# Kernel tuning notes

Hardware: AMD Instinct MI355X
Metric: run time of the kernel (lower is better)

## Reference

```python
import jax, jax.numpy as jnp
import numpy as np
from jax import lax

B_, N_, DIM, HID, DST, NT, IR, DTR, HH, WW = 16, 4096, 192, 384, 16, 17, 128, 24, 64, 64


def _selective_scan(u, delta, A, Bs, Cs, D, delta_bias):
    # u, delta: (B, Din, L); A: (Din, N); Bs, Cs: (B, N, L); D, delta_bias: (Din,)
    delta = jax.nn.softplus(delta + delta_bias[None, :, None])
    dT = jnp.moveaxis(delta, 2, 0)   # (L, B, Din)
    uT = jnp.moveaxis(u, 2, 0)       # (L, B, Din)
    BT = jnp.moveaxis(Bs, 2, 0)      # (L, B, N)
    CT = jnp.moveaxis(Cs, 2, 0)      # (L, B, N)
    Bsz, Din, L = u.shape
    Nst = A.shape[1]
    h0 = jnp.zeros((Bsz, Din, Nst), u.dtype)

    def step(h, inp):
        d_l, u_l, b_l, c_l = inp
        da = jnp.exp(d_l[:, :, None] * A[None])              # (B, Din, N)
        h = da * h + (d_l * u_l)[:, :, None] * b_l[:, None, :]
        y = jnp.einsum('bdn,bn->bd', h, c_l)
        return h, y

    _, ys = lax.scan(step, h0, (dT, uT, BT, CT))
    y = jnp.moveaxis(ys, 0, 2)                               # (B, Din, L)
    return y + u * D[None, :, None]


def _assm_forward(x, token_weight, gumbel_noise, embB, route_w1, route_b1, route_w2,
                  route_b2, inproj_w, inproj_b, cpe_w, cpe_b, x_proj_w, dt_w, dt_b,
                  A_logs, Ds, norm_g, norm_b, outproj_w, outproj_b, H, W, gather_type):
    B, n, C = x.shape
    hidden = inproj_w.shape[0]
    dst = token_weight.shape[1]
    dtr = dt_w.shape[1]

    # routing + gumbel-softmax (hard, straight-through)
    full_emb = embB @ token_weight                           # (NT, d_state)
    hmid = jax.nn.gelu(x @ route_w1.T + route_b1)
    logits = jax.nn.log_softmax(hmid @ route_w2.T + route_b2, axis=-1)
    y_soft = jax.nn.softmax(logits + gumbel_noise, axis=-1)
    idx = jnp.argmax(y_soft, axis=-1)                        # (B, n)
    y_hard = jax.nn.one_hot(idx, logits.shape[-1], dtype=y_soft.dtype)
    cls_policy = y_hard + y_soft - lax.stop_gradient(y_soft)
    prompt = cls_policy @ full_emb                           # (B, n, d_state)

    det = lax.stop_gradient(idx)
    # (gather_type 3/5 keypoint-group remap omitted: gather_type == 1 here)
    sort_idx = jnp.argsort(det, axis=-1)                     # (B, n)
    inv_idx = jnp.argsort(sort_idx, axis=-1)                 # index_reverse

    # in_proj (1x1 conv == pointwise linear) then depthwise CPE gate
    xi = x @ inproj_w.T + inproj_b                           # (B, n, hidden)
    xg = xi.reshape(B, H, W, hidden).transpose(0, 3, 1, 2)   # NCHW
    cpe = lax.conv_general_dilated(xg, cpe_w, (1, 1), 'SAME',
                                   feature_group_count=hidden,
                                   dimension_numbers=('NCHW', 'OIHW', 'NCHW'))
    cpe = cpe + cpe_b[None, :, None, None]
    xg = xg * jax.nn.sigmoid(cpe)
    xflat = xg.reshape(B, hidden, n).transpose(0, 2, 1)      # (B, n, hidden)

    sem_x = jnp.take_along_axis(xflat, sort_idx[:, :, None], axis=1)

    # Selective_Scan core
    xs = sem_x.transpose(0, 2, 1)                            # (B, Din, L)
    x_dbl = jnp.einsum('bdl,cd->bcl', xs, x_proj_w)          # (B, dtr+2N, L)
    dts, Bs, Cs = jnp.split(x_dbl, [dtr, dtr + dst], axis=1)
    dts = jnp.einsum('brl,dr->bdl', dts, dt_w)
    if gather_type != 0:
        Cs = Cs + prompt.transpose(0, 2, 1)
    A = -jnp.exp(A_logs)
    y = _selective_scan(xs, dts, A, Bs, Cs, Ds, dt_b)        # (B, Din, L)
    y = y.transpose(0, 2, 1)                                 # (B, L, hidden)

    mu = jnp.mean(y, axis=-1, keepdims=True)
    var = jnp.mean(jnp.square(y - mu), axis=-1, keepdims=True)
    yn = (y - mu) / jnp.sqrt(var + 1e-5) * norm_g + norm_b
    out = yn @ outproj_w.T + outproj_b                       # (B, n, dim)
    out = jnp.take_along_axis(out, inv_idx[:, :, None], axis=1)
    return out


def setup_inputs() -> dict:
    key = jax.random.key(0)
    ks = jax.random.split(key, 16)

    def rn(k, sh, s=0.02):
        return jax.random.normal(k, sh, dtype=jnp.float32) * s

    u = jax.random.uniform(ks[0], (B_, N_, NT), jnp.float32, 1e-6, 1.0 - 1e-6)
    gumbel = -jnp.log(-jnp.log(u))

    # faithful dt bias init (inverse-softplus of log-uniform dt)
    rng = np.random.default_rng(0)
    dt = np.exp(rng.uniform(size=HID) * (np.log(0.1) - np.log(0.001)) + np.log(0.001))
    dt = np.clip(dt, 1e-4, None)
    inv_dt = dt + np.log(-np.expm1(-dt))

    A_logs = jnp.log(jnp.tile(jnp.arange(1, DST + 1, dtype=jnp.float32), (HID, 1)))

    return {
        'x': jax.random.normal(ks[1], (B_, N_, DIM), jnp.float32),
        'token_weight': rn(ks[2], (IR, DST), 0.1),
        'gumbel_noise': gumbel,
        'embB': jax.random.uniform(ks[3], (NT, IR), jnp.float32, -1.0 / NT, 1.0 / NT),
        'route_w1': rn(ks[4], (DIM // 3, DIM)),
        'route_b1': jnp.zeros((DIM // 3,), jnp.float32),
        'route_w2': rn(ks[5], (NT, DIM // 3)),
        'route_b2': jnp.zeros((NT,), jnp.float32),
        'inproj_w': rn(ks[6], (HID, DIM)),
        'inproj_b': jnp.zeros((HID,), jnp.float32),
        'cpe_w': rn(ks[7], (HID, 1, 3, 3), 0.1),
        'cpe_b': jnp.zeros((HID,), jnp.float32),
        'x_proj_w': rn(ks[8], (DTR + 2 * DST, HID)),
        'dt_w': jax.random.uniform(ks[9], (HID, DTR), jnp.float32, -DTR ** -0.5, DTR ** -0.5),
        'dt_b': jnp.asarray(inv_dt, jnp.float32),
        'A_logs': A_logs,
        'Ds': jnp.ones((HID,), jnp.float32),
        'norm_g': jnp.ones((HID,), jnp.float32),
        'norm_b': jnp.zeros((HID,), jnp.float32),
        'outproj_w': rn(ks[10], (DIM, HID)),
        'outproj_b': jnp.zeros((DIM,), jnp.float32),
        'H': HH,
        'W': WW,
        'gather_type': 1,
    }


def reference(x, token_weight, gumbel_noise, embB, route_w1, route_b1, route_w2,
              route_b2, inproj_w, inproj_b, cpe_w, cpe_b, x_proj_w, dt_w, dt_b,
              A_logs, Ds, norm_g, norm_b, outproj_w, outproj_b, H, W, gather_type):
    return _assm_forward(x, token_weight, gumbel_noise, embB, route_w1, route_b1,
                         route_w2, route_b2, inproj_w, inproj_b, cpe_w, cpe_b,
                         x_proj_w, dt_w, dt_b, A_logs, Ds, norm_g, norm_b,
                         outproj_w, outproj_b, H, W, gather_type)
```

## Files before the change

kernel.cpp:

```cpp
#include <hip/hip_runtime.h>
#include <math.h>

#define NB 16
#define NL 4096
#define ND 192
#define NH 384
#define NS 16
#define NTK 17
#define NIR 128
#define NR 24
#define NHH 64
#define NWW 64
#define NCHUNKS 32
#define CHUNKLEN 128
#define NTOK (NB*NL)

typedef __attribute__((ext_vector_type(8))) short short8;
typedef __attribute__((ext_vector_type(4))) float floatx4;

__device__ __forceinline__ float gelu_tanh(float x){
  return 0.5f*x*(1.0f + tanhf(0.7978845608028654f*(x + 0.044715f*x*x*x)));
}
__device__ __forceinline__ float softplus_f(float x){
  return (x > 20.0f) ? x : log1pf(expf(x));
}
__device__ __forceinline__ short f2bf(float f){
  unsigned u = __float_as_uint(f);
  unsigned r = (u + 0x7fffu + ((u >> 16) & 1u)) >> 16;
  return (short)r;
}

union Pack8 { uint4 v; short s[8]; };

__global__ void k_cvtw(const float* __restrict__ inw, const float* __restrict__ ow,
                       const float* __restrict__ xpw, const float* __restrict__ dtw,
                       short* __restrict__ inwb, short* __restrict__ owb,
                       short* __restrict__ xpwb, short* __restrict__ dtwb,
                       const float* __restrict__ embB, const float* __restrict__ tw,
                       float* __restrict__ fe){
  int i = blockIdx.x*256 + threadIdx.x;
  int stride = gridDim.x*256;
  for (int p = i; p < NH*ND; p += stride) inwb[p] = f2bf(inw[p]);
  for (int p = i; p < ND*NH; p += stride) owb[p] = f2bf(ow[p]);
  for (int p = i; p < 56*NH; p += stride) xpwb[p] = f2bf(xpw[p]);
  for (int p = i; p < NH*32; p += stride){
    int r = p >> 5, c = p & 31;
    dtwb[p] = (c < NR) ? f2bf(dtw[r*NR + c]) : (short)0;
  }
  if (blockIdx.x == 0){
    for (int o = threadIdx.x; o < NTK*NS; o += 256){
      int t = o / NS, s = o % NS;
      float acc = 0.f;
      for (int k = 0; k < NIR; ++k) acc += embB[t*NIR+k]*tw[k*NS+s];
      fe[o] = acc;
    }
  }
}

template<int EPI>
__global__ __launch_bounds__(256) void k_gemm(const float* __restrict__ A, int lda,
    const float* __restrict__ W, int ldw, const float* __restrict__ bias,
    float* __restrict__ C, int ldc, int N, int K){
  __shared__ float As[16][68];
  __shared__ float Ws[16][68];
  int tid = threadIdx.x;
  int m0 = blockIdx.x*64, n0 = blockIdx.y*64;
  int tx = tid & 15, ty = tid >> 4;
  int srow = tid >> 2, skseg = (tid & 3)*4;
  float acc[4][4] = {};
  for (int k0 = 0; k0 < K; k0 += 16){
    {
      const float* ap = A + (size_t)(m0+srow)*lda + k0 + skseg;
      float4 v = *(const float4*)ap;
      As[skseg+0][srow]=v.x; As[skseg+1][srow]=v.y;
      As[skseg+2][srow]=v.z; As[skseg+3][srow]=v.w;
    }
    {
      float4 v = {0.f,0.f,0.f,0.f};
      if (n0 + srow < N) v = *(const float4*)(W + (size_t)(n0+srow)*ldw + k0 + skseg);
      Ws[skseg+0][srow]=v.x; Ws[skseg+1][srow]=v.y;
      Ws[skseg+2][srow]=v.z; Ws[skseg+3][srow]=v.w;
    }
    __syncthreads();
    #pragma unroll
    for (int kk = 0; kk < 16; ++kk){
      float4 av = *(const float4*)&As[kk][ty*4];
      float4 wv = *(const float4*)&Ws[kk][tx*4];
      acc[0][0] += av.x*wv.x; acc[0][1] += av.x*wv.y;
      acc[0][2] += av.x*wv.z; acc[0][3] += av.x*wv.w;
      acc[1][0] += av.y*wv.x; acc[1][1] += av.y*wv.y;
      acc[1][2] += av.y*wv.z; acc[1][3] += av.y*wv.w;
      acc[2][0] += av.z*wv.x; acc[2][1] += av.z*wv.y;
      acc[2][2] += av.z*wv.z; acc[2][3] += av.z*wv.w;
      acc[3][0] += av.w*wv.x; acc[3][1] += av.w*wv.y;
      acc[3][2] += av.w*wv.z; acc[3][3] += av.w*wv.w;
    }
    __syncthreads();
  }
  #pragma unroll
  for (int i = 0; i < 4; ++i){
    int m = m0 + ty*4 + i;
    #pragma unroll
    for (int j = 0; j < 4; ++j){
      int n = n0 + tx*4 + j;
      if (n < N){
        float v = acc[i][j] + (bias ? bias[n] : 0.f);
        if (EPI==1) v = gelu_tanh(v);
        C[(size_t)m*ldc + n] = v;
      }
    }
  }
}

template<int EPI, int AF32, int LNA>
__global__ __launch_bounds__(256) void k_mfma(const void* __restrict__ Aptr, int lda,
    const short* __restrict__ Wbf, int ldw, const float* __restrict__ bias,
    float* __restrict__ C, int ldc, int N, int K, const int* __restrict__ remap,
    const float* __restrict__ lnm, const float* __restrict__ lnr,
    const float* __restrict__ lng, const float* __restrict__ lnb){
  __shared__ short As[128*40];
  __shared__ short Bs[64*40];
  int tid = threadIdx.x;
  int m0 = blockIdx.x*128, n0 = blockIdx.y*64;
  int w = tid >> 6, lane = tid & 63;
  int lq = lane >> 4, lr = lane & 15;
  floatx4 acc[2][4];
  #pragma unroll
  for (int i = 0; i < 2; ++i)
    #pragma unroll
    for (int j = 0; j < 4; ++j) acc[i][j] = (floatx4){0.f,0.f,0.f,0.f};
  int ar = tid >> 1, aq = (tid & 1)*2;
  int br = tid >> 2, bq = tid & 3;
  float mr = 0.f, rr = 0.f;
  if (LNA){ mr = lnm[m0+ar]; rr = lnr[m0+ar]; }
  for (int k0 = 0; k0 < K; k0 += 32){
    Pack8 sa0, sa1;
    if (AF32){
      const float* ap = (const float*)Aptr + (size_t)(m0+ar)*lda + k0 + aq*8;
      float f[16];
      float4 f0 = *(const float4*)(ap);
      float4 f1 = *(const float4*)(ap+4);
      float4 f2 = *(const float4*)(ap+8);
      float4 f3 = *(const float4*)(ap+12);
      f[0]=f0.x; f[1]=f0.y; f[2]=f0.z; f[3]=f0.w;
      f[4]=f1.x; f[5]=f1.y; f[6]=f1.z; f[7]=f1.w;
      f[8]=f2.x; f[9]=f2.y; f[10]=f2.z; f[11]=f2.w;
      f[12]=f3.x; f[13]=f3.y; f[14]=f3.z; f[15]=f3.w;
      if (LNA){
        const float* gp = lng + k0 + aq*8;
        const float* bp = lnb + k0 + aq*8;
        #pragma unroll
        for (int j = 0; j < 16; ++j) f[j] = (f[j]-mr)*rr*gp[j] + bp[j];
      }
      #pragma unroll
      for (int j = 0; j < 8; ++j){ sa0.s[j] = f2bf(f[j]); sa1.s[j] = f2bf(f[8+j]); }
    } else {
      const short* ap = (const short*)Aptr + (size_t)(m0+ar)*lda + k0 + aq*8;
      sa0.v = *(const uint4*)ap;
      sa1.v = *(const uint4*)(ap + 8);
    }
    uint4 bv = {0u,0u,0u,0u};
    if (n0 + br < N) bv = *(const uint4*)(Wbf + (size_t)(n0+br)*ldw + k0 + bq*8);
    __syncthreads();
    *(uint4*)&As[ar*40 + aq*8]     = sa0.v;
    *(uint4*)&As[ar*40 + aq*8 + 8] = sa1.v;
    *(uint4*)&Bs[br*40 + bq*8]     = bv;
    __syncthreads();
    short8 a0 = *(const short8*)&As[(w*32      + lr)*40 + lq*8];
    short8 a1 = *(const short8*)&As[(w*32 + 16 + lr)*40 + lq*8];
    short8 b0 = *(const short8*)&Bs[(     lr)*40 + lq*8];
    short8 b1 = *(const short8*)&Bs[(16 + lr)*40 + lq*8];
    short8 b2 = *(const short8*)&Bs[(32 + lr)*40 + lq*8];
    short8 b3 = *(const short8*)&Bs[(48 + lr)*40 + lq*8];
    acc[0][0] = __builtin_amdgcn_mfma_f32_16x16x32_bf16(a0, b0, acc[0][0], 0,0,0);
    acc[0][1] = __builtin_amdgcn_mfma_f32_16x16x32_bf16(a0, b1, acc[0][1], 0,0,0);
    acc[0][2] = __builtin_amdgcn_mfma_f32_16x16x32_bf16(a0, b2, acc[0][2], 0,0,0);
    acc[0][3] = __builtin_amdgcn_mfma_f32_16x16x32_bf16(a0, b3, acc[0][3], 0,0,0);
    acc[1][0] = __builtin_amdgcn_mfma_f32_16x16x32_bf16(a1, b0, acc[1][0], 0,0,0);
    acc[1][1] = __builtin_amdgcn_mfma_f32_16x16x32_bf16(a1, b1, acc[1][1], 0,0,0);
    acc[1][2] = __builtin_amdgcn_mfma_f32_16x16x32_bf16(a1, b2, acc[1][2], 0,0,0);
    acc[1][3] = __builtin_amdgcn_mfma_f32_16x16x32_bf16(a1, b3, acc[1][3], 0,0,0);
  }
  #pragma unroll
  for (int mt = 0; mt < 2; ++mt){
    #pragma unroll
    for (int r = 0; r < 4; ++r){
      int m = m0 + w*32 + mt*16 + lq*4 + r;
      int orow = (EPI==3) ? remap[m] : m;
      #pragma unroll
      for (int nt = 0; nt < 4; ++nt){
        int n = n0 + nt*16 + lr;
        if (n < N){
          float v = acc[mt][nt][r] + (bias ? bias[n] : 0.f);
          if (EPI==2) v = softplus_f(v);
          C[(size_t)orow*ldc + n] = v;
        }
      }
    }
  }
}

__global__ __launch_bounds__(256) void k_argmax(const float* __restrict__ hmid,
    const float* __restrict__ w2, const float* __restrict__ b2,
    const float* __restrict__ gumbel, int* __restrict__ idx){
  int g = blockIdx.x*256 + threadIdx.x;
  float hm[64];
  const float4* hp = (const float4*)(hmid + (size_t)g*64);
  #pragma unroll
  for (int i = 0; i < 16; ++i){
    float4 v = hp[i];
    hm[i*4+0]=v.x; hm[i*4+1]=v.y; hm[i*4+2]=v.z; hm[i*4+3]=v.w;
  }
  float best = -INFINITY; int bi = 0;
  for (int c = 0; c < NTK; ++c){
    float s = b2[c] + gumbel[(size_t)g*NTK + c];
    #pragma unroll
    for (int j = 0; j < 64; ++j) s += hm[j]*w2[c*64+j];
    if (s > best){ best = s; bi = c; }
  }
  idx[g] = bi;
}

__global__ __launch_bounds__(256) void k_sort(const int* __restrict__ idx,
    int* __restrict__ rmap, int* __restrict__ inv){
  int b = blockIdx.x, t = threadIdx.x;
  __shared__ int hist[NTK][256];
  __shared__ int tot[NTK];
  __shared__ int keybase[NTK];
  int keys[16];
  const int* ip = idx + b*NL + t*16;
  #pragma unroll
  for (int i = 0; i < 16; ++i) keys[i] = ip[i];
  #pragma unroll
  for (int k = 0; k < NTK; ++k){
    int c = 0;
    #pragma unroll
    for (int i = 0; i < 16; ++i) c += (keys[i]==k) ? 1 : 0;
    hist[k][t] = c;
  }
  __syncthreads();
  if (t < NTK){
    int run = 0;
    for (int j = 0; j < 256; ++j){ int v = hist[t][j]; hist[t][j] = run; run += v; }
    tot[t] = run;
  }
  __syncthreads();
  if (t == 0){
    int base = 0;
    for (int k = 0; k < NTK; ++k){ keybase[k] = base; base += tot[k]; }
  }
  __syncthreads();
  #pragma unroll
  for (int i = 0; i < 16; ++i){
    int k = keys[i];
    int cb = 0;
    #pragma unroll
    for (int j = 0; j < 16; ++j) cb += (j < i && keys[j]==k) ? 1 : 0;
    int pos = keybase[k] + hist[k][t] + cb;
    rmap[b*NL + pos] = b*NL + t*16 + i;
    inv[b*NL + t*16 + i] = pos;
  }
}

__global__ __launch_bounds__(384) void k_cpe(const float* __restrict__ xi,
    const float* __restrict__ cw, const float* __restrict__ cb,
    const int* __restrict__ inv, float* __restrict__ us){
  int bl = blockIdx.x;
  int cg = bl & 3;
  int xt = (bl>>2) & 7;
  int yt = (bl>>5) & 7;
  int b  = bl >> 8;
  __shared__ float tile[10*10*96];
  int tx = threadIdx.x;
  int ty = threadIdx.y;
  int c0 = cg*96;
  int ch = c0 + tx;
  for (int yy = 0; yy < 10; ++yy){
    int gy = yt*8 + yy - 1;
    for (int xx = ty; xx < 10; xx += 4){
      int gx = xt*8 + xx - 1;
      float v = 0.f;
      if (gy >= 0 && gy < NHH && gx >= 0 && gx < NWW)
        v = xi[((size_t)(b*NL + gy*NWW + gx))*NH + ch];
      tile[(yy*10 + xx)*96 + tx] = v;
    }
  }
  float wreg[9];
  #pragma unroll
  for (int j = 0; j < 9; ++j) wreg[j] = cw[ch*9 + j];
  float bias = cb[ch];
  __syncthreads();
  for (int yy = ty; yy < 8; yy += 4){
    #pragma unroll
    for (int xx = 0; xx < 8; ++xx){
      float acc = bias;
      #pragma unroll
      for (int dy = 0; dy < 3; ++dy)
        #pragma unroll
        for (int dx = 0; dx < 3; ++dx)
          acc += tile[((yy+dy)*10 + (xx+dx))*96 + tx] * wreg[dy*3+dx];
      float center = tile[((yy+1)*10 + (xx+1))*96 + tx];
      float gate = 1.f/(1.f + expf(-acc));
      int l = (yt*8+yy)*NWW + xt*8+xx;
      int pos = inv[b*NL + l];
      us[((size_t)(b*NL + pos))*NH + ch] = center*gate;
    }
  }
}

__global__ __launch_bounds__(256) void k_bc(const float* __restrict__ dbl,
    const int* __restrict__ idx, const float* __restrict__ fe,
    const int* __restrict__ gt, float* __restrict__ Bsb, float* __restrict__ Csb,
    short* __restrict__ dtsb){
  int g = blockIdx.x*256 + threadIdx.x;
  const float* dr = dbl + (size_t)g*56;
  int id = idx[g];
  int gather = gt[0];
  #pragma unroll
  for (int n = 0; n < NR; ++n) dtsb[(size_t)g*32 + n] = f2bf(dr[n]);
  #pragma unroll
  for (int n = NR; n < 32; ++n) dtsb[(size_t)g*32 + n] = 0;
  #pragma unroll
  for (int n = 0; n < NS; ++n){
    Bsb[(size_t)g*NS + n] = dr[24+n];
    float c = dr[40+n];
    if (gather != 0) c += fe[id*NS + n];
    Csb[(size_t)g*NS + n] = c;
  }
}

__device__ __forceinline__ void decay16(bool pw, float dlt, const float* An, float* a){
  if (pw){
    float r  = __expf(dlt*An[0]);
    float r2 = r*r;
    float r3 = r2*r;
    float r4 = r2*r2;
    float r8 = r4*r4;
    float r12 = r8*r4;
    a[0]=r;     a[1]=r2;     a[2]=r3;     a[3]=r4;
    a[4]=r4*r;  a[5]=r4*r2;  a[6]=r4*r3;  a[7]=r8;
    a[8]=r8*r;  a[9]=r8*r2;  a[10]=r8*r3; a[11]=r12;
    a[12]=r12*r; a[13]=r12*r2; a[14]=r12*r3; a[15]=r8*r8;
  } else {
    #pragma unroll
    for (int n = 0; n < NS; ++n) a[n] = __expf(dlt*An[n]);
  }
}
__device__ __forceinline__ bool pwcheck(const float* An){
  bool pw = true;
  #pragma unroll
  for (int n = 1; n < NS; ++n)
    pw = pw && (fabsf(An[n] - (n+1)*An[0]) <= 1e-4f*fabsf(An[n]));
  return pw;
}

__global__ __launch_bounds__(384) void k_scan1(const float* __restrict__ delta,
    const float* __restrict__ us, const float* __restrict__ Bsb,
    const float* __restrict__ A_logs, float* __restrict__ sds, float* __restrict__ Boff){
  int bc = blockIdx.x;
  int c = bc & (NCHUNKS-1);
  int b = bc >> 5;
  int d = threadIdx.x;
  __shared__ float4 Bsh[CHUNKLEN*4];
  int base = b*NL + c*CHUNKLEN;
  {
    const float4* Bg = (const float4*)(Bsb + (size_t)base*NS);
    for (int p = d; p < CHUNKLEN*4; p += 384) Bsh[p] = Bg[p];
  }
  float An[NS];
  #pragma unroll
  for (int n = 0; n < NS; ++n) An[n] = -expf(A_logs[d*NS + n]);
  bool pw = pwcheck(An);
  float h[NS];
  #pragma unroll
  for (int n = 0; n < NS; ++n) h[n]=0.f;
  float sd = 0.f;
  __syncthreads();
  size_t gi = (size_t)base*NH + d;
  float dlt = delta[gi];
  float uv  = us[gi];
  #pragma unroll 2
  for (int s = 0; s < CHUNKLEN; ++s){
    float dltc = dlt, uvc = uv;
    if (s < CHUNKLEN-1){
      dlt = delta[gi + NH];
      uv  = us[gi + NH];
    }
    float du = dltc*uvc;
    sd += dltc;
    float a[NS];
    decay16(pw, dltc, An, a);
    float bb[NS];
    #pragma unroll
    for (int q = 0; q < 4; ++q) *(float4*)&bb[4*q] = Bsh[s*4 + q];
    #pragma unroll
    for (int n = 0; n < NS; ++n) h[n] = a[n]*h[n] + du*bb[n];
    gi += NH;
  }
  sds[(size_t)bc*NH + d] = sd;
  size_t o = ((size_t)bc*NH + d)*NS;
  *(float4*)(Boff + o)      = make_float4(h[0], h[1], h[2], h[3]);
  *(float4*)(Boff + o + 4)  = make_float4(h[4], h[5], h[6], h[7]);
  *(float4*)(Boff + o + 8)  = make_float4(h[8], h[9], h[10],h[11]);
  *(float4*)(Boff + o + 12) = make_float4(h[12],h[13],h[14],h[15]);
}

__global__ __launch_bounds__(256) void k_scan2(const float* __restrict__ A_logs,
    const float* __restrict__ sds, float* __restrict__ Boff){
  int i = blockIdx.x*256 + threadIdx.x;
  int dn = i % (NH*NS);
  int b = i / (NH*NS);
  float An = -expf(A_logs[dn]);
  int d = dn >> 4;
  float h = 0.f;
  for (int c = 0; c < NCHUNKS; ++c){
    int bc = b*NCHUNKS + c;
    float sd = sds[(size_t)bc*NH + d];
    float a = __expf(sd*An);
    size_t o = (size_t)bc*(NH*NS) + dn;
    float bo = Boff[o];
    Boff[o] = h;
    h = a*h + bo;
  }
}

__global__ __launch_bounds__(384) void k_scan3(const float* __restrict__ delta,
    const float* __restrict__ Bsb, const float* __restrict__ Csb,
    const float* __restrict__ A_logs, const float* __restrict__ Ds,
    const float* __restrict__ hinit, float* __restrict__ us){
  int bc = blockIdx.x;
  int c = bc & (NCHUNKS-1);
  int b = bc >> 5;
  int d = threadIdx.x;
  __shared__ float4 Bsh[CHUNKLEN*4];
  __shared__ float4 Csh[CHUNKLEN*4];
  int base = b*NL + c*CHUNKLEN;
  {
    const float4* Bg = (const float4*)(Bsb + (size_t)base*NS);
    const float4* Cg = (const float4*)(Csb + (size_t)base*NS);
    for (int p = d; p < CHUNKLEN*4; p += 384){
      Bsh[p] = Bg[p];
      Csh[p] = Cg[p];
    }
  }
  float An[NS];
  #pragma unroll
  for (int n = 0; n < NS; ++n) An[n] = -expf(A_logs[d*NS + n]);
  bool pw = pwcheck(An);
  float h[NS];
  size_t ho = ((size_t)bc*NH + d)*NS;
  {
    float4 h0 = *(const float4*)(hinit + ho);
    float4 h1 = *(const float4*)(hinit + ho + 4);
    float4 h2 = *(const float4*)(hinit + ho + 8);
    float4 h3 = *(const float4*)(hinit + ho + 12);
    h[0]=h0.x; h[1]=h0.y; h[2]=h0.z; h[3]=h0.w;
    h[4]=h1.x; h[5]=h1.y; h[6]=h1.z; h[7]=h1.w;
    h[8]=h2.x; h[9]=h2.y; h[10]=h2.z; h[11]=h2.w;
    h[12]=h3.x; h[13]=h3.y; h[14]=h3.z; h[15]=h3.w;
  }
  float Dd = Ds[d];
  __syncthreads();
  size_t gi = (size_t)base*NH + d;
  float dlt = delta[gi];
  float uv  = us[gi];
  #pragma unroll 2
  for (int s = 0; s < CHUNKLEN; ++s){
    float dltc = dlt, uvc = uv;
    if (s < CHUNKLEN-1){
      dlt = delta[gi + NH];
      uv  = us[gi + NH];
    }
    float du = dltc*uvc;
    float a[NS];
    decay16(pw, dltc, An, a);
    float bb[NS], cc[NS];
    #pragma unroll
    for (int q = 0; q < 4; ++q){
      *(float4*)&bb[4*q] = Bsh[s*4 + q];
      *(float4*)&cc[4*q] = Csh[s*4 + q];
    }
    #pragma unroll
    for (int n = 0; n < NS; ++n) h[n] = a[n]*h[n] + du*bb[n];
    float ya = 0.f, yb = 0.f, yc = 0.f, yd = 0.f;
    #pragma unroll
    for (int q = 0; q < 4; ++q){
      ya += h[q]*cc[q];
      yb += h[4+q]*cc[4+q];
      yc += h[8+q]*cc[8+q];
      yd += h[12+q]*cc[12+q];
    }
    float y = (ya+yb)+(yc+yd);
    us[gi] = y + uvc*Dd;
    gi += NH;
  }
}

__global__ __launch_bounds__(256) void k_lnstat(const float* __restrict__ y,
    float* __restrict__ mean, float* __restrict__ rstd){
  int g = blockIdx.x*4 + (threadIdx.x >> 6);
  int lane = threadIdx.x & 63;
  size_t ro = (size_t)g*NH;
  float v[6];
  #pragma unroll
  for (int i = 0; i < 6; ++i) v[i] = y[ro + i*64 + lane];
  float s = 0.f;
  #pragma unroll
  for (int i = 0; i < 6; ++i) s += v[i];
  #pragma unroll
  for (int off = 32; off > 0; off >>= 1) s += __shfl_xor(s, off);
  float mu = s * (1.f/NH);
  float vs = 0.f;
  #pragma unroll
  for (int i = 0; i < 6; ++i){ float d = v[i]-mu; vs += d*d; }
  #pragma unroll
  for (int off = 32; off > 0; off >>= 1) vs += __shfl_xor(vs, off);
  float rs = rsqrtf(vs*(1.f/NH) + 1e-5f);
  if (lane == 0){ mean[g] = mu; rstd[g] = rs; }
}

extern "C" void kernel_launch(void* const* d_in, const int* in_sizes, int n_in,
                              void* d_out, int out_size, void* d_ws, size_t ws_size,
                              hipStream_t stream){
  const float* x      = (const float*)d_in[0];
  const float* tw     = (const float*)d_in[1];
  const float* gumbel = (const float*)d_in[2];
  const float* embB   = (const float*)d_in[3];
  const float* rw1    = (const float*)d_in[4];
  const float* rb1    = (const float*)d_in[5];
  const float* rw2    = (const float*)d_in[6];
  const float* rb2    = (const float*)d_in[7];
  const float* inw    = (const float*)d_in[8];
  const float* inb    = (const float*)d_in[9];
  const float* cw     = (const float*)d_in[10];
  const float* cb     = (const float*)d_in[11];
  const float* xpw    = (const float*)d_in[12];
  const float* dtw    = (const float*)d_in[13];
  const float* dtb    = (const float*)d_in[14];
  const float* A_logs = (const float*)d_in[15];
  const float* Ds     = (const float*)d_in[16];
  const float* ng     = (const float*)d_in[17];
  const float* nbv    = (const float*)d_in[18];
  const float* ow     = (const float*)d_in[19];
  const float* ob     = (const float*)d_in[20];
  const int*   gt     = (const int*)d_in[23];
  float* out = (float*)d_out;

  float* ws = (float*)d_ws;
  size_t o = 0;
  float* fe   = ws + o; o += 512;
  int* idx    = (int*)(ws + o); o += NTOK;
  int* rmap   = (int*)(ws + o); o += NTOK;
  int* inv    = (int*)(ws + o); o += NTOK;
  float* hmid = ws + o; o += (size_t)NTOK*64;
  float* xi   = ws + o; o += (size_t)NTOK*NH;
  float* us   = ws + o; o += (size_t)NTOK*NH;
  float* Bsb  = ws + o; o += (size_t)NTOK*NS;
  float* Csb  = ws + o; o += (size_t)NTOK*NS;
  float* sds  = ws + o; o += (size_t)NB*NCHUNKS*NH;
  float* Bof  = ws + o; o += (size_t)NB*NCHUNKS*NH*NS;
  short* inwb = (short*)(ws + o); o += (NH*ND)/2;
  short* owb  = (short*)(ws + o); o += (ND*NH)/2;
  short* xpwb = (short*)(ws + o); o += (56*NH)/2 + 32;
  short* dtwb = (short*)(ws + o); o += (NH*32)/2;
  float* dbl = hmid;
  float* delta = xi;
  short* dtsb = (short*)Bof;
  float* lnmean = (float*)idx;
  float* lnrstd = (float*)inv;

  k_cvtw<<<64,256,0,stream>>>(inw, ow, xpw, dtw, inwb, owb, xpwb, dtwb, embB, tw, fe);
  k_gemm<1><<<dim3(NTOK/64,1),256,0,stream>>>(x, ND, rw1, ND, rb1, hmid, 64, 64, ND);
  k_argmax<<<NTOK/256,256,0,stream>>>(hmid, rw2, rb2, gumbel, idx);
  k_sort<<<NB,256,0,stream>>>(idx, rmap, inv);
  k_mfma<0,1,0><<<dim3(NTOK/128,6),256,0,stream>>>(x, ND, inwb, ND, inb, xi, NH, NH, ND,
      nullptr, nullptr, nullptr, nullptr, nullptr);
  k_cpe<<<NB*64*4,dim3(96,4),0,stream>>>(xi, cw, cb, inv, us);
  k_mfma<0,1,0><<<dim3(NTOK/128,1),256,0,stream>>>(us, NH, xpwb, NH, nullptr, dbl, 56, 56, NH,
      nullptr, nullptr, nullptr, nullptr, nullptr);
  k_bc<<<NTOK/256,256,0,stream>>>(dbl, idx, fe, gt, Bsb, Csb, dtsb);
  k_mfma<2,0,0><<<dim3(NTOK/128,6),256,0,stream>>>(dtsb, 32, dtwb, 32, dtb, delta, NH, NH, 32,
      nullptr, nullptr, nullptr, nullptr, nullptr);
  k_scan1<<<NB*NCHUNKS,384,0,stream>>>(delta, us, Bsb, A_logs, sds, Bof);
  k_scan2<<<(NB*NH*NS)/256,256,0,stream>>>(A_logs, sds, Bof);
  k_scan3<<<NB*NCHUNKS,384,0,stream>>>(delta, Bsb, Csb, A_logs, Ds, Bof, us);
  k_lnstat<<<NTOK/4,256,0,stream>>>(us, lnmean, lnrstd);
  k_mfma<3,1,1><<<dim3(NTOK/128,3),256,0,stream>>>(us, NH, owb, NH, ob, out, ND, ND, NH,
      rmap, lnmean, lnrstd, ng, nbv);
}
```

Baseline: 726.8 us.

## Fuse x_proj GEMM with B/C split and LayerNorm stats into scan

Replaces the generic x_proj MFMA GEMM plus the separate k_bc split kernel with one kernel that computes the 56-wide projection and writes dt (bf16), B and C (with the prompt embedding added) straight from the accumulators. It also moves the per-token LayerNorm mean/rstd computation into the tail of k_scan3, re-reading each chunk's freshly written rows after a block barrier. This removes two launches and the round trip of the intermediate dbl buffer. In exchange, k_scan3 gets a serial stats phase that runs on only 512 blocks, and the fused GEMM epilogue does scattered small stores.

```diff
diff --git a/kernel.cpp b/kernel.cpp
--- a/kernel.cpp
+++ b/kernel.cpp
@@ -200,6 +200,87 @@
   }
 }
 
+__global__ __launch_bounds__(256) void k_xdbl(const float* __restrict__ us,
+    const short* __restrict__ xpwb, const int* __restrict__ idx,
+    const float* __restrict__ fe, const int* __restrict__ gt,
+    float* __restrict__ Bsb, float* __restrict__ Csb, short* __restrict__ dtsb){
+  __shared__ short As[128*40];
+  __shared__ short Bs[64*40];
+  int tid = threadIdx.x;
+  int m0 = blockIdx.x*128;
+  int w = tid >> 6, lane = tid & 63;
+  int lq = lane >> 4, lr = lane & 15;
+  floatx4 acc[2][4];
+  #pragma unroll
+  for (int i = 0; i < 2; ++i)
+    #pragma unroll
+    for (int j = 0; j < 4; ++j) acc[i][j] = (floatx4){0.f,0.f,0.f,0.f};
+  int ar = tid >> 1, aq = (tid & 1)*2;
+  int br = tid >> 2, bq = tid & 3;
+  for (int k0 = 0; k0 < NH; k0 += 32){
+    Pack8 sa0, sa1;
+    {
+      const float* ap = us + (size_t)(m0+ar)*NH + k0 + aq*8;
+      float f[16];
+      float4 f0 = *(const float4*)(ap);
+      float4 f1 = *(const float4*)(ap+4);
+      float4 f2 = *(const float4*)(ap+8);
+      float4 f3 = *(const float4*)(ap+12);
+      f[0]=f0.x; f[1]=f0.y; f[2]=f0.z; f[3]=f0.w;
+      f[4]=f1.x; f[5]=f1.y; f[6]=f1.z; f[7]=f1.w;
+      f[8]=f2.x; f[9]=f2.y; f[10]=f2.z; f[11]=f2.w;
+      f[12]=f3.x; f[13]=f3.y; f[14]=f3.z; f[15]=f3.w;
+      #pragma unroll
+      for (int j = 0; j < 8; ++j){ sa0.s[j] = f2bf(f[j]); sa1.s[j] = f2bf(f[8+j]); }
+    }
+    uint4 bv = {0u,0u,0u,0u};
+    if (br < 56) bv = *(const uint4*)(xpwb + (size_t)br*NH + k0 + bq*8);
+    __syncthreads();
+    *(uint4*)&As[ar*40 + aq*8]     = sa0.v;
+    *(uint4*)&As[ar*40 + aq*8 + 8] = sa1.v;
+    *(uint4*)&Bs[br*40 + bq*8]     = bv;
+    __syncthreads();
+    short8 a0 = *(const short8*)&As[(w*32      + lr)*40 + lq*8];
+    short8 a1 = *(const short8*)&As[(w*32 + 16 + lr)*40 + lq*8];
+    short8 b0 = *(const short8*)&Bs[(     lr)*40 + lq*8];
+    short8 b1 = *(const short8*)&Bs[(16 + lr)*40 + lq*8];
+    short8 b2 = *(const short8*)&Bs[(32 + lr)*40 + lq*8];
+    short8 b3 = *(const short8*)&Bs[(48 + lr)*40 + lq*8];
+    acc[0][0] = __builtin_amdgcn_mfma_f32_16x16x32_bf16(a0, b0, acc[0][0], 0,0,0);
+    acc[0][1] = __builtin_amdgcn_mfma_f32_16x16x32_bf16(a0, b1, acc[0][1], 0,0,0);
+    acc[0][2] = __builtin_amdgcn_mfma_f32_16x16x32_bf16(a0, b2, acc[0][2], 0,0,0);
+    acc[0][3] = __builtin_amdgcn_mfma_f32_16x16x32_bf16(a0, b3, acc[0][3], 0,0,0);
+    acc[1][0] = __builtin_amdgcn_mfma_f32_16x16x32_bf16(a1, b0, acc[1][0], 0,0,0);
+    acc[1][1] = __builtin_amdgcn_mfma_f32_16x16x32_bf16(a1, b1, acc[1][1], 0,0,0);
+    acc[1][2] = __builtin_amdgcn_mfma_f32_16x16x32_bf16(a1, b2, acc[1][2], 0,0,0);
+    acc[1][3] = __builtin_amdgcn_mfma_f32_16x16x32_bf16(a1, b3, acc[1][3], 0,0,0);
+  }
+  int gather = gt[0];
+  #pragma unroll
+  for (int mt = 0; mt < 2; ++mt){
+    #pragma unroll
+    for (int r = 0; r < 4; ++r){
+      int m = m0 + w*32 + mt*16 + lq*4 + r;
+      int id = idx[m];
+      #pragma unroll
+      for (int nt = 0; nt < 4; ++nt){
+        int n = nt*16 + lr;
+        float v = acc[mt][nt][r];
+        if (n < 24){
+          dtsb[(size_t)m*32 + n] = f2bf(v);
+        } else if (n < 40){
+          Bsb[(size_t)m*NS + (n-24)] = v;
+          if (n < 32) dtsb[(size_t)m*32 + n] = 0;
+        } else if (n < 56){
+          float cv = v;
+          if (gather != 0) cv += fe[id*NS + (n-40)];
+          Csb[(size_t)m*NS + (n-40)] = cv;
+        }
+      }
+    }
+  }
+}
+
 __global__ __launch_bounds__(256) void k_argmax(const float* __restrict__ hmid,
     const float* __restrict__ w2, const float* __restrict__ b2,
     const float* __restrict__ gumbel, int* __restrict__ idx){
@@ -308,27 +389,6 @@
   }
 }
 
-__global__ __launch_bounds__(256) void k_bc(const float* __restrict__ dbl,
-    const int* __restrict__ idx, const float* __restrict__ fe,
-    const int* __restrict__ gt, float* __restrict__ Bsb, float* __restrict__ Csb,
-    short* __restrict__ dtsb){
-  int g = blockIdx.x*256 + threadIdx.x;
-  const float* dr = dbl + (size_t)g*56;
-  int id = idx[g];
-  int gather = gt[0];
-  #pragma unroll
-  for (int n = 0; n < NR; ++n) dtsb[(size_t)g*32 + n] = f2bf(dr[n]);
-  #pragma unroll
-  for (int n = NR; n < 32; ++n) dtsb[(size_t)g*32 + n] = 0;
-  #pragma unroll
-  for (int n = 0; n < NS; ++n){
-    Bsb[(size_t)g*NS + n] = dr[24+n];
-    float c = dr[40+n];
-    if (gather != 0) c += fe[id*NS + n];
-    Csb[(size_t)g*NS + n] = c;
-  }
-}
-
 __device__ __forceinline__ void decay16(bool pw, float dlt, const float* An, float* a){
   if (pw){
     float r  = __expf(dlt*An[0]);
@@ -427,7 +487,8 @@
 __global__ __launch_bounds__(384) void k_scan3(const float* __restrict__ delta,
     const float* __restrict__ Bsb, const float* __restrict__ Csb,
     const float* __restrict__ A_logs, const float* __restrict__ Ds,
-    const float* __restrict__ hinit, float* __restrict__ us){
+    const float* __restrict__ hinit, float* __restrict__ us,
+    float* __restrict__ lnmean, float* __restrict__ lnrstd){
   int bc = blockIdx.x;
   int c = bc & (NCHUNKS-1);
   int b = bc >> 5;
@@ -494,29 +555,30 @@
     us[gi] = y + uvc*Dd;
     gi += NH;
   }
-}
-
-__global__ __launch_bounds__(256) void k_lnstat(const float* __restrict__ y,
-    float* __restrict__ mean, float* __restrict__ rstd){
-  int g = blockIdx.x*4 + (threadIdx.x >> 6);
-  int lane = threadIdx.x & 63;
-  size_t ro = (size_t)g*NH;
-  float v[6];
-  #pragma unroll
-  for (int i = 0; i < 6; ++i) v[i] = y[ro + i*64 + lane];
-  float s = 0.f;
-  #pragma unroll
-  for (int i = 0; i < 6; ++i) s += v[i];
-  #pragma unroll
-  for (int off = 32; off > 0; off >>= 1) s += __shfl_xor(s, off);
-  float mu = s * (1.f/NH);
-  float vs = 0.f;
-  #pragma unroll
-  for (int i = 0; i < 6; ++i){ float d = v[i]-mu; vs += d*d; }
-  #pragma unroll
-  for (int off = 32; off > 0; off >>= 1) vs += __shfl_xor(vs, off);
-  float rs = rsqrtf(vs*(1.f/NH) + 1e-5f);
-  if (lane == 0){ mean[g] = mu; rstd[g] = rs; }
+  __syncthreads();
+  {
+    int w = d >> 6, lane = d & 63;
+    for (int t = w; t < CHUNKLEN; t += 6){
+      int row = base + t;
+      const float* rp = us + (size_t)row*NH;
+      float v[6];
+      #pragma unroll
+      for (int i = 0; i < 6; ++i) v[i] = rp[i*64 + lane];
+      float s = 0.f;
+      #pragma unroll
+      for (int i = 0; i < 6; ++i) s += v[i];
+      #pragma unroll
+      for (int off = 32; off > 0; off >>= 1) s += __shfl_xor(s, off);
+      float mu = s * (1.f/NH);
+      float vs = 0.f;
+      #pragma unroll
+      for (int i = 0; i < 6; ++i){ float dv = v[i]-mu; vs += dv*dv; }
+      #pragma unroll
+      for (int off = 32; off > 0; off >>= 1) vs += __shfl_xor(vs, off);
+      float rs = rsqrtf(vs*(1.f/NH) + 1e-5f);
+      if (lane == 0){ lnmean[row] = mu; lnrstd[row] = rs; }
+    }
+  }
 }
 
 extern "C" void kernel_launch(void* const* d_in, const int* in_sizes, int n_in,
@@ -563,7 +625,6 @@
   short* owb  = (short*)(ws + o); o += (ND*NH)/2;
   short* xpwb = (short*)(ws + o); o += (56*NH)/2 + 32;
   short* dtwb = (short*)(ws + o); o += (NH*32)/2;
-  float* dbl = hmid;
   float* delta = xi;
   short* dtsb = (short*)Bof;
   float* lnmean = (float*)idx;
@@ -576,15 +637,13 @@
   k_mfma<0,1,0><<<dim3(NTOK/128,6),256,0,stream>>>(x, ND, inwb, ND, inb, xi, NH, NH, ND,
       nullptr, nullptr, nullptr, nullptr, nullptr);
   k_cpe<<<NB*64*4,dim3(96,4),0,stream>>>(xi, cw, cb, inv, us);
-  k_mfma<0,1,0><<<dim3(NTOK/128,1),256,0,stream>>>(us, NH, xpwb, NH, nullptr, dbl, 56, 56, NH,
-      nullptr, nullptr, nullptr, nullptr, nullptr);
-  k_bc<<<NTOK/256,256,0,stream>>>(dbl, idx, fe, gt, Bsb, Csb, dtsb);
+  k_xdbl<<<NTOK/128,256,0,stream>>>(us, xpwb, idx, fe, gt, Bsb, Csb, dtsb);
   k_mfma<2,0,0><<<dim3(NTOK/128,6),256,0,stream>>>(dtsb, 32, dtwb, 32, dtb, delta, NH, NH, 32,
       nullptr, nullptr, nullptr, nullptr, nullptr);
   k_scan1<<<NB*NCHUNKS,384,0,stream>>>(delta, us, Bsb, A_logs, sds, Bof);
   k_scan2<<<(NB*NH*NS)/256,256,0,stream>>>(A_logs, sds, Bof);
-  k_scan3<<<NB*NCHUNKS,384,0,stream>>>(delta, Bsb, Csb, A_logs, Ds, Bof, us);
-  k_lnstat<<<NTOK/4,256,0,stream>>>(us, lnmean, lnrstd);
+  k_scan3<<<NB*NCHUNKS,384,0,stream>>>(delta, Bsb, Csb, A_logs, Ds, Bof, us,
+                                       lnmean, lnrstd);
   k_mfma<3,1,1><<<dim3(NTOK/128,3),256,0,stream>>>(us, NH, owb, NH, ob, out, ND, ND, NH,
       rmap, lnmean, lnrstd, ng, nbv);
 }
```

Result: faster. 689.8 us (-5.1%).
